# Optimization experiments

Measured on AMD Instinct MI355X. Metric: run time of the kernel, lower is better.

## Reference

```python
import jax, jax.numpy as jnp
import numpy as np

HEADS = 16
DIM_HEAD = 64
RMS_EPS = 1.1920929e-07  # torch.finfo(float32).eps (torch RMSNorm eps=None default)
ROPE_THETA = 10000.0


def _rope(x):
    # x: [b, h, n, d]; rotary-embedding-torch style interleaved rotation
    n, d = x.shape[-2], x.shape[-1]
    inv_freq = 1.0 / (ROPE_THETA ** (jnp.arange(0, d, 2, dtype=jnp.float32) / d))
    t = jnp.arange(n, dtype=jnp.float32)
    freqs = t[:, None] * inv_freq[None, :]              # [n, d/2]
    cos = jnp.repeat(jnp.cos(freqs), 2, axis=-1)        # [n, d] interleaved
    sin = jnp.repeat(jnp.sin(freqs), 2, axis=-1)
    x1 = x[..., ::2]
    x2 = x[..., 1::2]
    rot = jnp.stack((-x2, x1), axis=-1).reshape(x.shape)  # rotate_half, interleaved pairs
    return x * cos + rot * sin


def setup_inputs() -> dict:
    key = jax.random.key(0)
    ks = jax.random.split(key, 6)
    b, n, dim = 2, 2048, 1024
    tokens = jax.random.normal(ks[0], (b, n, dim), dtype=jnp.float32)
    norm_weight = jnp.ones((dim,), dtype=jnp.float32)
    wq = jax.random.normal(ks[1], (dim, dim), dtype=jnp.float32) * 0.02
    wk = jax.random.normal(ks[2], (dim, dim), dtype=jnp.float32) * 0.02
    wv = jax.random.normal(ks[3], (dim, dim), dtype=jnp.float32) * 0.02
    wo = jax.random.normal(ks[4], (dim, dim), dtype=jnp.float32) * 0.02
    return {"tokens": tokens, "norm_weight": norm_weight, "wq": wq, "wk": wk, "wv": wv, "wo": wo}


def reference(tokens, norm_weight, wq, wk, wv, wo):
    b, n, dim = tokens.shape
    # RMSNorm (elementwise affine)
    x = tokens * jax.lax.rsqrt(jnp.mean(tokens * tokens, axis=-1, keepdims=True) + RMS_EPS)
    x = x * norm_weight
    # QKV projections (torch Linear: x @ W.T), split heads: b n (h d) -> b h n d
    def split(y):
        return y.reshape(b, n, HEADS, DIM_HEAD).transpose(0, 2, 1, 3)
    q = split(x @ wq.T) * (DIM_HEAD ** -0.5)
    k = split(x @ wk.T)
    v = split(x @ wv.T)
    # rotary embedding (no kv cache -> same positions for q and k)
    q = _rope(q)
    k = _rope(k)
    sim = jnp.einsum('bhid,bhjd->bhij', q, k)
    causal = jnp.triu(jnp.ones((n, n), dtype=bool), k=1)
    sim = jnp.where(causal, -jnp.finfo(sim.dtype).max, sim)
    attn = jax.nn.softmax(sim, axis=-1)
    out = jnp.einsum('bhij,bhjd->bhid', attn, v)
    out = out.transpose(0, 2, 1, 3).reshape(b, n, dim)  # merge heads
    return out @ wo.T
```

## Files before the change

### kernel.cpp

```cpp
#include <hip/hip_runtime.h>

typedef __bf16 bf16x8 __attribute__((ext_vector_type(8)));
typedef float f32x4 __attribute__((ext_vector_type(4)));

#define DIM 1024
#define NSEQ 2048

#define GL2LDS(g, l) __builtin_amdgcn_global_load_lds( \
    (const __attribute__((address_space(1))) void*)(g), \
    (__attribute__((address_space(3))) void*)(l), 16, 0, 0)

#define MFMA16(a, b, c) __builtin_amdgcn_mfma_f32_16x16x32_bf16(a, b, c, 0, 0, 0)

__global__ __launch_bounds__(256) void cvt_kernel(const float* __restrict__ s,
                                                  __bf16* __restrict__ d) {
    int i = (blockIdx.x * 256 + threadIdx.x) * 4;
    float4 f = *(const float4*)(s + i);
    union { uint2 u; __bf16 h[4]; } p;
    p.h[0] = (__bf16)f.x; p.h[1] = (__bf16)f.y;
    p.h[2] = (__bf16)f.z; p.h[3] = (__bf16)f.w;
    *(uint2*)(d + i) = p.u;
}

__global__ __launch_bounds__(256) void cvt3_kernel(const float* __restrict__ wq,
                                                   const float* __restrict__ wk,
                                                   const float* __restrict__ wv,
                                                   __bf16* __restrict__ dq,
                                                   __bf16* __restrict__ dk,
                                                   __bf16* __restrict__ dv,
                                                   int* __restrict__ counters) {
    if (blockIdx.x == 0 && blockIdx.y == 0 && threadIdx.x < 8)
        counters[threadIdx.x] = 0;
    const float* s = blockIdx.y == 0 ? wq : (blockIdx.y == 1 ? wk : wv);
    __bf16*      d = blockIdx.y == 0 ? dq : (blockIdx.y == 1 ? dk : dv);
    int i = (blockIdx.x * 256 + threadIdx.x) * 4;
    float4 f = *(const float4*)(s + i);
    union { uint2 u; __bf16 h[4]; } p;
    p.h[0] = (__bf16)f.x; p.h[1] = (__bf16)f.y;
    p.h[2] = (__bf16)f.z; p.h[3] = (__bf16)f.w;
    *(uint2*)(d + i) = p.u;
}

__global__ __launch_bounds__(256) void rmsnorm_kernel(const float* __restrict__ x,
                                                      const float* __restrict__ g,
                                                      __bf16* __restrict__ o) {
    int row = blockIdx.x;
    int t = threadIdx.x;
    float4 xv = ((const float4*)(x + (size_t)row * DIM))[t];
    float ss = xv.x*xv.x + xv.y*xv.y + xv.z*xv.z + xv.w*xv.w;
    #pragma unroll
    for (int off = 32; off; off >>= 1) ss += __shfl_xor(ss, off, 64);
    __shared__ float red[4];
    if ((t & 63) == 0) red[t >> 6] = ss;
    __syncthreads();
    ss = red[0] + red[1] + red[2] + red[3];
    float r = rsqrtf(ss * (1.0f / 1024.0f) + 1.1920929e-07f);
    float4 gv = ((const float4*)g)[t];
    union { uint2 u; __bf16 h[4]; } p;
    p.h[0] = (__bf16)(xv.x * r * gv.x);
    p.h[1] = (__bf16)(xv.y * r * gv.y);
    p.h[2] = (__bf16)(xv.z * r * gv.z);
    p.h[3] = (__bf16)(xv.w * r * gv.w);
    *(uint2*)(o + (size_t)row * DIM + t * 4) = p.u;
}

__global__ __launch_bounds__(256) void rope_kernel(__bf16* __restrict__ qb,
                                                   __bf16* __restrict__ kb) {
    int bid = blockIdx.x;
    __bf16* x = (bid & 1) ? kb : qb;
    int gid = (bid >> 1) * 256 + threadIdx.x;
    int row = gid >> 9;
    int pr = gid & 511;
    int pos = row & (NSEQ - 1);
    int dp = pr & 31;
    float inv = __expf(-(float)dp * (9.210340371976184f / 32.0f));
    float ang = (float)pos * inv;
    float sn, cs;
    sincosf(ang, &sn, &cs);
    size_t off = (size_t)row * DIM + pr * 2;
    union { unsigned int u; __bf16 h[2]; } p;
    p.u = *(const unsigned int*)(x + off);
    float x1 = (float)p.h[0], x2 = (float)p.h[1];
    p.h[0] = (__bf16)(x1 * cs - x2 * sn);
    p.h[1] = (__bf16)(x2 * cs + x1 * sn);
    *(unsigned int*)(x + off) = p.u;
}

template <typename CT>
__device__ __forceinline__ void gemm_body(const __bf16* __restrict__ A,
                                          const __bf16* __restrict__ B,
                                          CT* __restrict__ C,
                                          int mb, int nb, int ldc, float scale,
                                          __bf16* As, __bf16* Bs) {
    int t = threadIdx.x;
    int w = t >> 6, l = t & 63;
    int wm = (w >> 1) * 64, wn = (w & 1) * 64;
    int lrow = l & 15, lq = l >> 4;
    f32x4 acc[4][4] = {};

    int srow = w * 32 + (l >> 3);
    int sc8 = (l & 7) * 8;
    const __bf16* gA = A + (size_t)(mb * 128 + srow) * 1024 + sc8;
    const __bf16* gB = B + (size_t)(nb * 128 + srow) * 1024 + sc8;
    __bf16* lA = As + (size_t)(w * 32) * 64;
    __bf16* lB = Bs + (size_t)(w * 32) * 64;

    for (int kt = 0; kt < 16; ++kt) {
        int k0 = kt * 64;
        #pragma unroll
        for (int c = 0; c < 4; ++c) {
            GL2LDS(gA + (size_t)c * 8 * 1024 + k0, lA + c * 8 * 64);
            GL2LDS(gB + (size_t)c * 8 * 1024 + k0, lB + c * 8 * 64);
        }
        __syncthreads();
        #pragma unroll
        for (int ch = 0; ch < 2; ++ch) {
            bf16x8 af[4], bfr[4];
            #pragma unroll
            for (int i = 0; i < 4; ++i)
                af[i] = *(const bf16x8*)&As[(wm + i * 16 + lrow) * 64 + ch * 32 + lq * 8];
            #pragma unroll
            for (int i = 0; i < 4; ++i)
                bfr[i] = *(const bf16x8*)&Bs[(wn + i * 16 + lrow) * 64 + ch * 32 + lq * 8];
            #pragma unroll
            for (int rt = 0; rt < 4; ++rt)
                #pragma unroll
                for (int ct = 0; ct < 4; ++ct)
                    acc[rt][ct] = MFMA16(af[rt], bfr[ct], acc[rt][ct]);
        }
        __syncthreads();
    }
    #pragma unroll
    for (int rt = 0; rt < 4; ++rt)
        #pragma unroll
        for (int ct = 0; ct < 4; ++ct)
            #pragma unroll
            for (int r = 0; r < 4; ++r) {
                int row = mb * 128 + wm + rt * 16 + lq * 4 + r;
                int col = nb * 128 + wn + ct * 16 + lrow;
                C[(size_t)row * ldc + col] = (CT)(acc[rt][ct][r] * scale);
            }
}

__global__ __launch_bounds__(256) void qkv_kernel(const __bf16* __restrict__ x,
                                                  const __bf16* __restrict__ wq,
                                                  const __bf16* __restrict__ wk,
                                                  const __bf16* __restrict__ wv,
                                                  __bf16* __restrict__ qb,
                                                  __bf16* __restrict__ kb,
                                                  __bf16* __restrict__ vtb) {
    __shared__ __bf16 As[128 * 64];
    __shared__ __bf16 Bs[128 * 64];
    int bm = blockIdx.x, bn = blockIdx.y, z = blockIdx.z;
    if (z == 0)      gemm_body<__bf16>(x,  wq, qb,  bm, bn, 1024,
                                       0.125f * 1.44269504088896340736f, As, Bs);
    else if (z == 1) gemm_body<__bf16>(x,  wk, kb,  bm, bn, 1024, 1.0f,   As, Bs);
    else             gemm_body<__bf16>(wv, x,  vtb, bn, bm, 4096, 1.0f,   As, Bs);
}

__global__ __launch_bounds__(256) void wo_kernel(const __bf16* __restrict__ A,
                                                 const __bf16* __restrict__ B,
                                                 float* __restrict__ C) {
    __shared__ __bf16 As[128 * 64];
    __shared__ __bf16 Bs[128 * 64];
    gemm_body<float>(A, B, C, blockIdx.x, blockIdx.y, 1024, 1.0f, As, Bs);
}

__global__ __launch_bounds__(256, 3) void attn_kernel(const __bf16* __restrict__ q,
                                                      const __bf16* __restrict__ kk,
                                                      const __bf16* __restrict__ vt,
                                                      __bf16* __restrict__ o,
                                                      int* __restrict__ counters) {
    int xcd = blockIdx.x & 7;
    int t = threadIdx.x;
    int w = t >> 6, l = t & 63;
    int lrow = l & 15, lq = l >> 4;
    int rw = (w & 1) * 32;
    int par = w >> 1;
    int row0 = t >> 3;
    int cb = t & 7;

    __shared__ __bf16 Kt[2][64 * 64];
    __shared__ __bf16 Vs[2][64 * 64];
    __shared__ __bf16 Ps[4][32 * 72];
    __shared__ int s_item;
    __bf16* pw = Ps[w];

    for (;;) {
        if (t == 0) s_item = atomicAdd(&counters[xcd], 1);
        __syncthreads();
        int item = s_item;
        if (item >= 128) break;
        int iq = 31 - (item >> 2);
        int bh = xcd * 4 + (item & 3);
        int h = bh & 15;
        int b = bh >> 4;
        int rowbase = b * NSEQ;

        const __bf16* kbase = kk + (size_t)rowbase * DIM + h * 64;
        const __bf16* vbase = vt + (size_t)(h * 64) * 4096 + b * 2048;

        bf16x8 qf[2][2];
        #pragma unroll
        for (int g = 0; g < 2; ++g) {
            const __bf16* qp = q + (size_t)(rowbase + iq * 64 + rw + g * 16 + lrow) * DIM + h * 64;
            qf[g][0] = *(const bf16x8*)(qp + lq * 8);
            qf[g][1] = *(const bf16x8*)(qp + 32 + lq * 8);
        }

        f32x4 oacc[2][4] = {};
        float m_r[2] = {-1e30f, -1e30f};
        float l_r[2] = {0.0f, 0.0f};

        const __bf16* kg = kbase + (size_t)row0 * DIM + cb * 8;
        const __bf16* vg = vbase + (size_t)row0 * 4096 + cb * 8;
        int dsw0 = (row0 * 8 + (cb ^ (row0 & 7))) * 8;
        int dsw1 = ((row0 + 32) * 8 + (cb ^ (row0 & 7))) * 8;

        uint4 k0a, k0b, v0a, v0b, k1a, k1b, v1a, v1b;
        k0a = *(const uint4*)(kg);
        k0b = *(const uint4*)(kg + (size_t)32 * DIM);
        v0a = *(const uint4*)(vg);
        v0b = *(const uint4*)(vg + (size_t)32 * 4096);
        if (iq >= 1) {
            k1a = *(const uint4*)(kg + (size_t)64 * DIM);
            k1b = *(const uint4*)(kg + (size_t)96 * DIM);
            v1a = *(const uint4*)(vg + 64);
            v1b = *(const uint4*)(vg + (size_t)32 * 4096 + 64);
        }
        *(uint4*)&Kt[0][dsw0] = k0a; *(uint4*)&Kt[0][dsw1] = k0b;
        *(uint4*)&Vs[0][dsw0] = v0a; *(uint4*)&Vs[0][dsw1] = v0b;
        if (iq >= 1) {
            *(uint4*)&Kt[1][dsw0] = k1a; *(uint4*)&Kt[1][dsw1] = k1b;
            *(uint4*)&Vs[1][dsw0] = v1a; *(uint4*)&Vs[1][dsw1] = v1b;
        }
        __syncthreads();

        int R = (iq + 2) >> 1;
        for (int rd = 0; rd < R; ++rd) {
            int jt = 2 * rd + par;
            bool pf = (rd + 1 < R);
            if (pf) {
                int je = 2 * rd + 2;
                size_t ko = (size_t)je * 64 * DIM;
                k0a = *(const uint4*)(kg + ko);
                k0b = *(const uint4*)(kg + ko + (size_t)32 * DIM);
                v0a = *(const uint4*)(vg + je * 64);
                v0b = *(const uint4*)(vg + (size_t)32 * 4096 + je * 64);
                if (je + 1 <= iq) {
                    k1a = *(const uint4*)(kg + ko + (size_t)64 * DIM);
                    k1b = *(const uint4*)(kg + ko + (size_t)96 * DIM);
                    v1a = *(const uint4*)(vg + je * 64 + 64);
                    v1b = *(const uint4*)(vg + (size_t)32 * 4096 + je * 64 + 64);
                }
            }
            if (jt <= iq) {
                const __bf16* Kb = Kt[par];
                const __bf16* Vb = Vs[par];
                int sw = lrow & 7;
                f32x4 st[2][4];
                #pragma unroll
                for (int ct = 0; ct < 4; ++ct) {
                    int rr = (ct * 16 + lrow) * 8;
                    bf16x8 ka0 = *(const bf16x8*)&Kb[(rr + (lq ^ sw)) * 8];
                    bf16x8 ka1 = *(const bf16x8*)&Kb[(rr + ((4 + lq) ^ sw)) * 8];
                    #pragma unroll
                    for (int g = 0; g < 2; ++g) {
                        f32x4 z = {};
                        z = MFMA16(ka0, qf[g][0], z);
                        z = MFMA16(ka1, qf[g][1], z);
                        st[g][ct] = z;
                    }
                }
                if (jt == iq) {
                    #pragma unroll
                    for (int g = 0; g < 2; ++g) {
                        int qrel = rw + g * 16 + lrow;
                        #pragma unroll
                        for (int ct = 0; ct < 4; ++ct)
                            #pragma unroll
                            for (int r = 0; r < 4; ++r)
                                if (ct * 16 + lq * 4 + r > qrel) st[g][ct][r] = -3.0e38f;
                    }
                }
                #pragma unroll
                for (int g = 0; g < 2; ++g) {
                    float m0 = fmaxf(fmaxf(st[g][0][0], st[g][0][1]), fmaxf(st[g][0][2], st[g][0][3]));
                    float m1 = fmaxf(fmaxf(st[g][1][0], st[g][1][1]), fmaxf(st[g][1][2], st[g][1][3]));
                    float m2 = fmaxf(fmaxf(st[g][2][0], st[g][2][1]), fmaxf(st[g][2][2], st[g][2][3]));
                    float m3 = fmaxf(fmaxf(st[g][3][0], st[g][3][1]), fmaxf(st[g][3][2], st[g][3][3]));
                    float mx = fmaxf(fmaxf(m0, m1), fmaxf(m2, m3));
                    mx = fmaxf(mx, __shfl_xor(mx, 16, 64));
                    mx = fmaxf(mx, __shfl_xor(mx, 32, 64));
                    if (!__all(mx - m_r[g] <= 8.0f)) {
                        float mnew = fmaxf(m_r[g], mx);
                        float alpha = __builtin_amdgcn_exp2f(m_r[g] - mnew);
                        l_r[g] *= alpha;
                        #pragma unroll
                        for (int ct = 0; ct < 4; ++ct)
                            #pragma unroll
                            for (int r = 0; r < 4; ++r) oacc[g][ct][r] *= alpha;
                        m_r[g] = mnew;
                    }
                    float ps = 0.0f;
                    #pragma unroll
                    for (int ct = 0; ct < 4; ++ct)
                        #pragma unroll
                        for (int r = 0; r < 4; ++r) {
                            float p = __builtin_amdgcn_exp2f(st[g][ct][r] - m_r[g]);
                            st[g][ct][r] = p;
                            ps += p;
                        }
                    ps += __shfl_xor(ps, 16, 64);
                    ps += __shfl_xor(ps, 32, 64);
                    l_r[g] += ps;
                }
                #pragma unroll
                for (int g = 0; g < 2; ++g)
                    #pragma unroll
                    for (int ct = 0; ct < 4; ++ct) {
                        union { uint2 u; __bf16 h4[4]; } pk;
                        #pragma unroll
                        for (int r = 0; r < 4; ++r) pk.h4[r] = (__bf16)st[g][ct][r];
                        *(uint2*)&pw[(g * 16 + lrow) * 72 + ct * 16 + lq * 4] = pk.u;
                    }
                bf16x8 pb[2][2];
                #pragma unroll
                for (int g = 0; g < 2; ++g) {
                    pb[g][0] = *(const bf16x8*)&pw[(g * 16 + lrow) * 72 + lq * 8];
                    pb[g][1] = *(const bf16x8*)&pw[(g * 16 + lrow) * 72 + 32 + lq * 8];
                }
                #pragma unroll
                for (int ct = 0; ct < 4; ++ct) {
                    int rr = (ct * 16 + lrow) * 8;
                    bf16x8 va0 = *(const bf16x8*)&Vb[(rr + (lq ^ sw)) * 8];
                    bf16x8 va1 = *(const bf16x8*)&Vb[(rr + ((4 + lq) ^ sw)) * 8];
                    #pragma unroll
                    for (int g = 0; g < 2; ++g) {
                        oacc[g][ct] = MFMA16(va0, pb[g][0], oacc[g][ct]);
                        oacc[g][ct] = MFMA16(va1, pb[g][1], oacc[g][ct]);
                    }
                }
            }
            if (pf) {
                __syncthreads();
                *(uint4*)&Kt[0][dsw0] = k0a; *(uint4*)&Kt[0][dsw1] = k0b;
                *(uint4*)&Vs[0][dsw0] = v0a; *(uint4*)&Vs[0][dsw1] = v0b;
                if (2 * rd + 3 <= iq) {
                    *(uint4*)&Kt[1][dsw0] = k1a; *(uint4*)&Kt[1][dsw1] = k1b;
                    *(uint4*)&Vs[1][dsw0] = v1a; *(uint4*)&Vs[1][dsw1] = v1b;
                }
                __syncthreads();
            }
        }

        __syncthreads();
        float* sc = (float*)&Ps[0][0];
        float* base = sc + (w & 1) * 2304 + l * 36;
        if (par == 1) {
            #pragma unroll
            for (int g = 0; g < 2; ++g)
                #pragma unroll
                for (int ct = 0; ct < 4; ++ct)
                    *(f32x4*)(base + g * 16 + ct * 4) = oacc[g][ct];
            base[32] = m_r[0]; base[33] = m_r[1];
            base[34] = l_r[0]; base[35] = l_r[1];
        }
        __syncthreads();
        if (par == 0) {
            #pragma unroll
            for (int g = 0; g < 2; ++g) {
                float mb = base[32 + g], lb = base[34 + g];
                float m = fmaxf(m_r[g], mb);
                float a  = __builtin_amdgcn_exp2f(m_r[g] - m);
                float bb = __builtin_amdgcn_exp2f(mb - m);
                float rcp = 1.0f / (a * l_r[g] + bb * lb);
                const size_t orow = (size_t)(rowbase + iq * 64 + rw + g * 16 + lrow) * DIM + h * 64;
                #pragma unroll
                for (int ct = 0; ct < 4; ++ct) {
                    f32x4 ob = *(const f32x4*)(base + g * 16 + ct * 4);
                    union { uint2 u; __bf16 h4[4]; } pk;
                    #pragma unroll
                    for (int r = 0; r < 4; ++r)
                        pk.h4[r] = (__bf16)((a * oacc[g][ct][r] + bb * ob[r]) * rcp);
                    *(uint2*)(o + orow + ct * 16 + lq * 4) = pk.u;
                }
            }
        }
    }
}

extern "C" void kernel_launch(void* const* d_in, const int* in_sizes, int n_in,
                              void* d_out, int out_size, void* d_ws, size_t ws_size,
                              hipStream_t stream) {
    const float* tokens = (const float*)d_in[0];
    const float* gamma  = (const float*)d_in[1];
    const float* wq = (const float*)d_in[2];
    const float* wk = (const float*)d_in[3];
    const float* wv = (const float*)d_in[4];
    const float* wo = (const float*)d_in[5];

    __bf16* ws  = (__bf16*)d_ws;
    __bf16* x   = ws;
    __bf16* qb  = x   + (size_t)4096 * 1024;
    __bf16* kb  = qb  + (size_t)4096 * 1024;
    __bf16* vtb = kb  + (size_t)4096 * 1024;
    __bf16* ao  = x;
    __bf16* wob = qb;
    float*  out = (float*)d_out;

    __bf16* wqb = (__bf16*)d_out;
    __bf16* wkb = wqb + (size_t)1024 * 1024;
    __bf16* wvb = wkb + (size_t)1024 * 1024;
    int* counters = (int*)((char*)d_out + (size_t)8 * 1024 * 1024);

    cvt3_kernel<<<dim3(1024, 3), 256, 0, stream>>>(wq, wk, wv, wqb, wkb, wvb, counters);

    rmsnorm_kernel<<<4096, 256, 0, stream>>>(tokens, gamma, x);

    qkv_kernel<<<dim3(32, 8, 3), 256, 0, stream>>>(x, wqb, wkb, wvb, qb, kb, vtb);

    rope_kernel<<<16384, 256, 0, stream>>>(qb, kb);

    attn_kernel<<<768, 256, 0, stream>>>(qb, kb, vtb, ao, counters);

    cvt_kernel<<<1024, 256, 0, stream>>>(wo, wob);

    wo_kernel<<<dim3(32, 8), 256, 0, stream>>>(ao, wob, out);
}
```

Measured before the change: 201.8 us.

## Fuse weight conversion, RMSNorm and rope table; fold rope into QKV epilogue

Weight conversion, RMSNorm and a precomputed cos/sin table now come from a single pre-kernel. Rope moves into the QKV GEMM epilogue using a lane shuffle and the table, so the separate read-modify-write rope pass over q/k goes away. The output projection uses 128x64 tiles to launch twice as many blocks, and the attention MFMA sections are wrapped in s_setprio to favour matrix issue. The trade-off is extra work and table loads in the GEMM epilogue, and a table buffer placed inside the output scratch area.

```diff
diff --git a/kernel.cpp b/kernel.cpp
--- a/kernel.cpp
+++ b/kernel.cpp
@@ -22,76 +22,65 @@
     *(uint2*)(d + i) = p.u;
 }
 
-__global__ __launch_bounds__(256) void cvt3_kernel(const float* __restrict__ wq,
-                                                   const float* __restrict__ wk,
-                                                   const float* __restrict__ wv,
-                                                   __bf16* __restrict__ dq,
-                                                   __bf16* __restrict__ dk,
-                                                   __bf16* __restrict__ dv,
-                                                   int* __restrict__ counters) {
-    if (blockIdx.x == 0 && blockIdx.y == 0 && threadIdx.x < 8)
-        counters[threadIdx.x] = 0;
-    const float* s = blockIdx.y == 0 ? wq : (blockIdx.y == 1 ? wk : wv);
-    __bf16*      d = blockIdx.y == 0 ? dq : (blockIdx.y == 1 ? dk : dv);
-    int i = (blockIdx.x * 256 + threadIdx.x) * 4;
-    float4 f = *(const float4*)(s + i);
-    union { uint2 u; __bf16 h[4]; } p;
-    p.h[0] = (__bf16)f.x; p.h[1] = (__bf16)f.y;
-    p.h[2] = (__bf16)f.z; p.h[3] = (__bf16)f.w;
-    *(uint2*)(d + i) = p.u;
-}
-
-__global__ __launch_bounds__(256) void rmsnorm_kernel(const float* __restrict__ x,
-                                                      const float* __restrict__ g,
-                                                      __bf16* __restrict__ o) {
-    int row = blockIdx.x;
+__global__ __launch_bounds__(256) void pre_kernel(const float* __restrict__ wq,
+                                                  const float* __restrict__ wk,
+                                                  const float* __restrict__ wv,
+                                                  __bf16* __restrict__ dq,
+                                                  __bf16* __restrict__ dk,
+                                                  __bf16* __restrict__ dv,
+                                                  float2* __restrict__ tbl,
+                                                  int* __restrict__ counters,
+                                                  const float* __restrict__ x,
+                                                  const float* __restrict__ g,
+                                                  __bf16* __restrict__ xo) {
+    int bid = blockIdx.x;
     int t = threadIdx.x;
-    float4 xv = ((const float4*)(x + (size_t)row * DIM))[t];
-    float ss = xv.x*xv.x + xv.y*xv.y + xv.z*xv.z + xv.w*xv.w;
-    #pragma unroll
-    for (int off = 32; off; off >>= 1) ss += __shfl_xor(ss, off, 64);
-    __shared__ float red[4];
-    if ((t & 63) == 0) red[t >> 6] = ss;
-    __syncthreads();
-    ss = red[0] + red[1] + red[2] + red[3];
-    float r = rsqrtf(ss * (1.0f / 1024.0f) + 1.1920929e-07f);
-    float4 gv = ((const float4*)g)[t];
-    union { uint2 u; __bf16 h[4]; } p;
-    p.h[0] = (__bf16)(xv.x * r * gv.x);
-    p.h[1] = (__bf16)(xv.y * r * gv.y);
-    p.h[2] = (__bf16)(xv.z * r * gv.z);
-    p.h[3] = (__bf16)(xv.w * r * gv.w);
-    *(uint2*)(o + (size_t)row * DIM + t * 4) = p.u;
-}
-
-__global__ __launch_bounds__(256) void rope_kernel(__bf16* __restrict__ qb,
-                                                   __bf16* __restrict__ kb) {
-    int bid = blockIdx.x;
-    __bf16* x = (bid & 1) ? kb : qb;
-    int gid = (bid >> 1) * 256 + threadIdx.x;
-    int row = gid >> 9;
-    int pr = gid & 511;
-    int pos = row & (NSEQ - 1);
-    int dp = pr & 31;
-    float inv = __expf(-(float)dp * (9.210340371976184f / 32.0f));
-    float ang = (float)pos * inv;
-    float sn, cs;
-    sincosf(ang, &sn, &cs);
-    size_t off = (size_t)row * DIM + pr * 2;
-    union { unsigned int u; __bf16 h[2]; } p;
-    p.u = *(const unsigned int*)(x + off);
-    float x1 = (float)p.h[0], x2 = (float)p.h[1];
-    p.h[0] = (__bf16)(x1 * cs - x2 * sn);
-    p.h[1] = (__bf16)(x2 * cs + x1 * sn);
-    *(unsigned int*)(x + off) = p.u;
-}
-
-template <typename CT>
+    if (bid == 0 && t < 8) counters[t] = 0;
+    if (bid < 3072) {
+        int slice = bid >> 10;
+        const float* s = slice == 0 ? wq : (slice == 1 ? wk : wv);
+        __bf16*      d = slice == 0 ? dq : (slice == 1 ? dk : dv);
+        int i = ((bid & 1023) * 256 + t) * 4;
+        float4 f = *(const float4*)(s + i);
+        union { uint2 u; __bf16 h[4]; } p;
+        p.h[0] = (__bf16)f.x; p.h[1] = (__bf16)f.y;
+        p.h[2] = (__bf16)f.z; p.h[3] = (__bf16)f.w;
+        *(uint2*)(d + i) = p.u;
+    } else if (bid < 3328) {
+        int e = (bid - 3072) * 256 + t;
+        int pos = e >> 5, dp = e & 31;
+        float inv = __expf(-(float)dp * (9.210340371976184f / 32.0f));
+        float sn, cs;
+        sincosf((float)pos * inv, &sn, &cs);
+        tbl[e] = make_float2(cs, sn);
+    } else {
+        int row = bid - 3328;
+        float4 xv = ((const float4*)(x + (size_t)row * DIM))[t];
+        float ss = xv.x*xv.x + xv.y*xv.y + xv.z*xv.z + xv.w*xv.w;
+        #pragma unroll
+        for (int off = 32; off; off >>= 1) ss += __shfl_xor(ss, off, 64);
+        __shared__ float red[4];
+        if ((t & 63) == 0) red[t >> 6] = ss;
+        __syncthreads();
+        ss = red[0] + red[1] + red[2] + red[3];
+        float r = rsqrtf(ss * (1.0f / 1024.0f) + 1.1920929e-07f);
+        float4 gv = ((const float4*)g)[t];
+        union { uint2 u; __bf16 h[4]; } p;
+        p.h[0] = (__bf16)(xv.x * r * gv.x);
+        p.h[1] = (__bf16)(xv.y * r * gv.y);
+        p.h[2] = (__bf16)(xv.z * r * gv.z);
+        p.h[3] = (__bf16)(xv.w * r * gv.w);
+        *(uint2*)(xo + (size_t)row * DIM + t * 4) = p.u;
+    }
+}
+
+template <typename CT, bool ROPE>
 __device__ __forceinline__ void gemm_body(const __bf16* __restrict__ A,
                                           const __bf16* __restrict__ B,
                                           CT* __restrict__ C,
                                           int mb, int nb, int ldc, float scale,
-                                          __bf16* As, __bf16* Bs) {
+                                          __bf16* As, __bf16* Bs,
+                                          const float2* __restrict__ tbl) {
     int t = threadIdx.x;
     int w = t >> 6, l = t & 63;
     int wm = (w >> 1) * 64, wn = (w & 1) * 64;
@@ -133,13 +122,22 @@
     #pragma unroll
     for (int rt = 0; rt < 4; ++rt)
         #pragma unroll
-        for (int ct = 0; ct < 4; ++ct)
+        for (int ct = 0; ct < 4; ++ct) {
+            int colg = nb * 128 + wn + ct * 16 + lrow;
+            int dp = ((ct * 16 + lrow) & 63) >> 1;
             #pragma unroll
             for (int r = 0; r < 4; ++r) {
-                int row = mb * 128 + wm + rt * 16 + lq * 4 + r;
-                int col = nb * 128 + wn + ct * 16 + lrow;
-                C[(size_t)row * ldc + col] = (CT)(acc[rt][ct][r] * scale);
-            }
+                int rowg = mb * 128 + wm + rt * 16 + lq * 4 + r;
+                float v = acc[rt][ct][r] * scale;
+                if constexpr (ROPE) {
+                    float p = __shfl_xor(v, 1, 64);
+                    float2 cs = tbl[((rowg & (NSEQ - 1)) << 5) + dp];
+                    v = (lrow & 1) ? (v * cs.x + p * cs.y)
+                                   : (v * cs.x - p * cs.y);
+                }
+                C[(size_t)rowg * ldc + colg] = (CT)v;
+            }
+        }
 }
 
 __global__ __launch_bounds__(256) void qkv_kernel(const __bf16* __restrict__ x,
@@ -148,22 +146,73 @@
                                                   const __bf16* __restrict__ wv,
                                                   __bf16* __restrict__ qb,
                                                   __bf16* __restrict__ kb,
-                                                  __bf16* __restrict__ vtb) {
+                                                  __bf16* __restrict__ vtb,
+                                                  const float2* __restrict__ tbl) {
     __shared__ __bf16 As[128 * 64];
     __shared__ __bf16 Bs[128 * 64];
     int bm = blockIdx.x, bn = blockIdx.y, z = blockIdx.z;
-    if (z == 0)      gemm_body<__bf16>(x,  wq, qb,  bm, bn, 1024,
-                                       0.125f * 1.44269504088896340736f, As, Bs);
-    else if (z == 1) gemm_body<__bf16>(x,  wk, kb,  bm, bn, 1024, 1.0f,   As, Bs);
-    else             gemm_body<__bf16>(wv, x,  vtb, bn, bm, 4096, 1.0f,   As, Bs);
+    if (z == 0)      gemm_body<__bf16, true >(x,  wq, qb,  bm, bn, 1024,
+                                       0.125f * 1.44269504088896340736f, As, Bs, tbl);
+    else if (z == 1) gemm_body<__bf16, true >(x,  wk, kb,  bm, bn, 1024, 1.0f, As, Bs, tbl);
+    else             gemm_body<__bf16, false>(wv, x,  vtb, bn, bm, 4096, 1.0f, As, Bs, tbl);
 }
 
 __global__ __launch_bounds__(256) void wo_kernel(const __bf16* __restrict__ A,
                                                  const __bf16* __restrict__ B,
                                                  float* __restrict__ C) {
     __shared__ __bf16 As[128 * 64];
-    __shared__ __bf16 Bs[128 * 64];
-    gemm_body<float>(A, B, C, blockIdx.x, blockIdx.y, 1024, 1.0f, As, Bs);
+    __shared__ __bf16 Bs[64 * 64];
+    int mb = blockIdx.x, nb = blockIdx.y;
+    int t = threadIdx.x;
+    int w = t >> 6, l = t & 63;
+    int wm = (w >> 1) * 64, wn = (w & 1) * 32;
+    int lrow = l & 15, lq = l >> 4;
+    f32x4 acc[4][2] = {};
+
+    int srowA = w * 32 + (l >> 3);
+    int srowB = w * 16 + (l >> 3);
+    int sc8 = (l & 7) * 8;
+    const __bf16* gA = A + (size_t)(mb * 128 + srowA) * 1024 + sc8;
+    const __bf16* gB = B + (size_t)(nb * 64 + srowB) * 1024 + sc8;
+    __bf16* lA = As + (size_t)(w * 32) * 64;
+    __bf16* lB = Bs + (size_t)(w * 16) * 64;
+
+    for (int kt = 0; kt < 16; ++kt) {
+        int k0 = kt * 64;
+        #pragma unroll
+        for (int c = 0; c < 4; ++c)
+            GL2LDS(gA + (size_t)c * 8 * 1024 + k0, lA + c * 8 * 64);
+        #pragma unroll
+        for (int c = 0; c < 2; ++c)
+            GL2LDS(gB + (size_t)c * 8 * 1024 + k0, lB + c * 8 * 64);
+        __syncthreads();
+        #pragma unroll
+        for (int ch = 0; ch < 2; ++ch) {
+            bf16x8 af[4], bfr[2];
+            #pragma unroll
+            for (int i = 0; i < 4; ++i)
+                af[i] = *(const bf16x8*)&As[(wm + i * 16 + lrow) * 64 + ch * 32 + lq * 8];
+            #pragma unroll
+            for (int i = 0; i < 2; ++i)
+                bfr[i] = *(const bf16x8*)&Bs[(wn + i * 16 + lrow) * 64 + ch * 32 + lq * 8];
+            #pragma unroll
+            for (int rt = 0; rt < 4; ++rt)
+                #pragma unroll
+                for (int ct = 0; ct < 2; ++ct)
+                    acc[rt][ct] = MFMA16(af[rt], bfr[ct], acc[rt][ct]);
+        }
+        __syncthreads();
+    }
+    #pragma unroll
+    for (int rt = 0; rt < 4; ++rt)
+        #pragma unroll
+        for (int ct = 0; ct < 2; ++ct)
+            #pragma unroll
+            for (int r = 0; r < 4; ++r) {
+                int row = mb * 128 + wm + rt * 16 + lq * 4 + r;
+                int col = nb * 64 + wn + ct * 16 + lrow;
+                C[(size_t)row * 1024 + col] = acc[rt][ct][r];
+            }
 }
 
 __global__ __launch_bounds__(256, 3) void attn_kernel(const __bf16* __restrict__ q,
@@ -259,6 +308,7 @@
                 const __bf16* Vb = Vs[par];
                 int sw = lrow & 7;
                 f32x4 st[2][4];
+                __builtin_amdgcn_s_setprio(1);
                 #pragma unroll
                 for (int ct = 0; ct < 4; ++ct) {
                     int rr = (ct * 16 + lrow) * 8;
@@ -272,6 +322,7 @@
                         st[g][ct] = z;
                     }
                 }
+                __builtin_amdgcn_s_setprio(0);
                 if (jt == iq) {
                     #pragma unroll
                     for (int g = 0; g < 2; ++g) {
@@ -330,6 +381,7 @@
                     pb[g][0] = *(const bf16x8*)&pw[(g * 16 + lrow) * 72 + lq * 8];
                     pb[g][1] = *(const bf16x8*)&pw[(g * 16 + lrow) * 72 + 32 + lq * 8];
                 }
+                __builtin_amdgcn_s_setprio(1);
                 #pragma unroll
                 for (int ct = 0; ct < 4; ++ct) {
                     int rr = (ct * 16 + lrow) * 8;
@@ -341,6 +393,7 @@
                         oacc[g][ct] = MFMA16(va1, pb[g][1], oacc[g][ct]);
                     }
                 }
+                __builtin_amdgcn_s_setprio(0);
             }
             if (pf) {
                 __syncthreads();
@@ -412,19 +465,17 @@
     __bf16* wqb = (__bf16*)d_out;
     __bf16* wkb = wqb + (size_t)1024 * 1024;
     __bf16* wvb = wkb + (size_t)1024 * 1024;
+    float2* tbl = (float2*)((char*)d_out + (size_t)6 * 1024 * 1024);
     int* counters = (int*)((char*)d_out + (size_t)8 * 1024 * 1024);
 
-    cvt3_kernel<<<dim3(1024, 3), 256, 0, stream>>>(wq, wk, wv, wqb, wkb, wvb, counters);
-
-    rmsnorm_kernel<<<4096, 256, 0, stream>>>(tokens, gamma, x);
-
-    qkv_kernel<<<dim3(32, 8, 3), 256, 0, stream>>>(x, wqb, wkb, wvb, qb, kb, vtb);
-
-    rope_kernel<<<16384, 256, 0, stream>>>(qb, kb);
+    pre_kernel<<<7424, 256, 0, stream>>>(wq, wk, wv, wqb, wkb, wvb, tbl, counters,
+                                         tokens, gamma, x);
+
+    qkv_kernel<<<dim3(32, 8, 3), 256, 0, stream>>>(x, wqb, wkb, wvb, qb, kb, vtb, tbl);
 
     attn_kernel<<<768, 256, 0, stream>>>(qb, kb, vtb, ao, counters);
 
     cvt_kernel<<<1024, 256, 0, stream>>>(wo, wob);
 
-    wo_kernel<<<dim3(32, 8), 256, 0, stream>>>(ao, wob, out);
-}
+    wo_kernel<<<dim3(32, 16), 256, 0, stream>>>(ao, wob, out);
+}
```

Result: no change. 203.3 us (+0.8%).
